# Optimization experiments

Measured on AMD Instinct MI355X. Metric: run time of the kernel, lower is better.

Reference implementation:

```python
import jax, jax.numpy as jnp
import numpy as np

N = 50000      # n_nodes
E = 800000     # n_edges (avg degree 16)
D_IN, D_HID, D_OUT = 128, 128, 64


def setup_inputs() -> dict:
    key = jax.random.key(0)
    ks = jax.random.split(key, 6)
    x = jax.random.normal(ks[0], (N, D_IN), dtype=jnp.float32)
    edge_index = jax.random.randint(ks[1], (2, E), 0, N, dtype=jnp.int32)
    # GCNConv params (glorot-ish scale), bias enabled by default in PyG
    W1 = jax.random.normal(ks[2], (D_IN, D_HID), dtype=jnp.float32) * (1.0 / np.sqrt(D_IN))
    b1 = jnp.zeros((D_HID,), dtype=jnp.float32)
    W2 = jax.random.normal(ks[3], (D_HID, D_OUT), dtype=jnp.float32) * (1.0 / np.sqrt(D_HID))
    b2 = jnp.zeros((D_OUT,), dtype=jnp.float32)
    return {"x": x, "edge_index": edge_index, "W1": W1, "b1": b1, "W2": W2, "b2": b2}


def _gcn_conv(x, src, dst, W, b):
    """PyG GCNConv: linear transform, add self-loops (weight 1),
    symmetric D^-1/2 A D^-1/2 aggregation (source->target), add bias."""
    xw = x @ W                                                # [N, Dout]
    ones = jnp.ones(dst.shape[0], dtype=xw.dtype)
    deg = jax.ops.segment_sum(ones, dst, num_segments=N) + 1.0  # +1 self-loop
    dis = jax.lax.rsqrt(deg)                                  # deg >= 1
    norm = dis[src] * dis[dst]                                # [E]
    msg = xw[src] * norm[:, None]                             # gather + scale
    agg = jax.ops.segment_sum(msg, dst, num_segments=N)       # scatter-add
    agg = agg + xw * (dis * dis)[:, None]                     # self-loop term
    return agg + b


def reference(x, edge_index, W1, b1, W2, b2):
    src, dst = edge_index[0], edge_index[1]
    z = jax.nn.relu(_gcn_conv(x, src, dst, W1, b1))
    z = _gcn_conv(z, src, dst, W2, b2)
    return z
```

## Files before the change

### kernel.cpp

```cpp
#include <hip/hip_runtime.h>

#define NN 50000
#define NE 800000
#define NB 196
#define BCAP 4608
#define KPAD 136
#define WSLAB (2 * 64 * KPAD)
#define CHUNKS 782

typedef __bf16 bf16x8 __attribute__((ext_vector_type(8)));
typedef float  f32x4  __attribute__((ext_vector_type(4)));

static __device__ __forceinline__ float bf2f(unsigned short h){
  union { unsigned u; float f; } c; c.u = ((unsigned)h) << 16; return c.f;
}
static __device__ __forceinline__ unsigned short f2bf(float f){
  union { float f; unsigned u; } c; c.f = f;
  unsigned u = c.u;
  return (unsigned short)((u + 0x7fffu + ((u >> 16) & 1u)) >> 16);
}
static __device__ __forceinline__ void split8(const float* f, bf16x8& hi, bf16x8& lo){
  #pragma unroll
  for (int j = 0; j < 8; j++){
    __bf16 h = (__bf16)f[j];
    hi[j] = h;
    lo[j] = (__bf16)(f[j] - (float)h);
  }
}
static __device__ __forceinline__ void addu4(float* a, uint4 w){
  a[0] += bf2f((unsigned short)(w.x & 0xffffu)); a[1] += bf2f((unsigned short)(w.x >> 16));
  a[2] += bf2f((unsigned short)(w.y & 0xffffu)); a[3] += bf2f((unsigned short)(w.y >> 16));
  a[4] += bf2f((unsigned short)(w.z & 0xffffu)); a[5] += bf2f((unsigned short)(w.z >> 16));
  a[6] += bf2f((unsigned short)(w.w & 0xffffu)); a[7] += bf2f((unsigned short)(w.w >> 16));
}

__global__ __launch_bounds__(256) void k_prep(const float* __restrict__ W1,
    const float* __restrict__ W2, unsigned short* __restrict__ wbuf,
    int* __restrict__ gcur){
  int s = blockIdx.x;
  if (s == 3){
    if (threadIdx.x < NB) gcur[threadIdx.x] = 0;
    return;
  }
  const float* W = (s < 2) ? W1 : W2;
  int ldw = (s < 2) ? 128 : 64;
  int coff = (s == 1) ? 64 : 0;
  unsigned short* wh = wbuf + (size_t)s * WSLAB;
  unsigned short* wl = wh + 64 * KPAD;
  for (int i = threadIdx.x; i < 128 * 64; i += 256){
    int k = i >> 6, n = i & 63;
    float v = W[(size_t)k * ldw + coff + n];
    unsigned short h = f2bf(v);
    unsigned short l = f2bf(v - bf2f(h));
    wh[n * KPAD + k] = h;
    wl[n * KPAD + k] = l;
  }
}

__global__ __launch_bounds__(256) void k_bfill(const int* __restrict__ src,
    const int* __restrict__ dst, int* __restrict__ gcur, unsigned* __restrict__ stg){
  __shared__ int lcnt[NB];
  __shared__ int gbase[NB];
  for (int i = threadIdx.x; i < NB; i += 256) lcnt[i] = 0;
  __syncthreads();
  int per = (NE + gridDim.x - 1) / gridDim.x;
  int e0 = blockIdx.x * per, e1 = min(e0 + per, NE);
  for (int e = e0 + threadIdx.x; e < e1; e += 256)
    atomicAdd(&lcnt[dst[e] >> 8], 1);
  __syncthreads();
  for (int b = threadIdx.x; b < NB; b += 256){
    gbase[b] = atomicAdd(&gcur[b], lcnt[b]);
    lcnt[b] = 0;
  }
  __syncthreads();
  for (int e = e0 + threadIdx.x; e < e1; e += 256){
    int d = dst[e];
    int b = d >> 8;
    unsigned entry = (unsigned)src[e] | (((unsigned)d & 255u) << 16);
    int pos = gbase[b] + atomicAdd(&lcnt[b], 1);
    if (pos < BCAP) stg[(size_t)b * BCAP + pos] = entry;
  }
}

__global__ __launch_bounds__(256) void k_build(const unsigned* __restrict__ stg,
    const int* __restrict__ gcur, int* __restrict__ rowstart, int* __restrict__ cnt,
    float* __restrict__ dis, int* __restrict__ csr){
  __shared__ int lcnt[256];
  __shared__ int sm[256];
  const int b = blockIdx.x;
  const int t = threadIdx.x;
  const int ecnt = min(gcur[b], BCAP);
  const int ebase = b * BCAP;
  lcnt[t] = 0;
  __syncthreads();
  for (int i = t; i < ecnt; i += 256){
    unsigned en = stg[ebase + i];
    atomicAdd(&lcnt[(en >> 16) & 255u], 1);
  }
  __syncthreads();
  int v = lcnt[t];
  sm[t] = v;
  __syncthreads();
  #pragma unroll
  for (int off = 1; off < 256; off <<= 1){
    int x = (t >= off) ? sm[t - off] : 0;
    __syncthreads();
    sm[t] += x;
    __syncthreads();
  }
  const int loff = sm[t] - v;
  const int node = (b << 8) + t;
  if (node < NN){
    rowstart[node] = ebase + loff;
    cnt[node] = v;
    dis[node] = rsqrtf((float)v + 1.0f);
  }
  __syncthreads();
  lcnt[t] = loff;
  __syncthreads();
  for (int i = t; i < ecnt; i += 256){
    unsigned en = stg[ebase + i];
    int pos = atomicAdd(&lcnt[(en >> 16) & 255u], 1);
    csr[ebase + pos] = (int)(en & 0xffffu);
  }
}

__global__ __launch_bounds__(256) void k_gemm1(const float* __restrict__ X,
    const unsigned short* __restrict__ wbuf, const float* __restrict__ dis,
    unsigned short* __restrict__ Y){
  const int t = threadIdx.x;
  const int wv = t >> 6;
  const int lane = t & 63;
  const int m = lane & 15;
  const int quad = lane >> 4;
  const int R0 = blockIdx.x * 64;
  const int row = R0 + wv * 16 + m;
  const int rowc = min(row, NN - 1);
  const float* pX = X + (size_t)rowc * 128 + quad * 8;

  f32x4 acc[8];
  #pragma unroll
  for (int tt = 0; tt < 8; tt++) acc[tt] = (f32x4){0.f, 0.f, 0.f, 0.f};

  #pragma unroll
  for (int ki = 0; ki < 4; ki++){
    float a[8];
    *(float4*)(a)     = *(const float4*)(pX + ki * 32);
    *(float4*)(a + 4) = *(const float4*)(pX + ki * 32 + 4);
    bf16x8 ah, al;
    split8(a, ah, al);
    #pragma unroll
    for (int tt = 0; tt < 8; tt++){
      const unsigned short* bp = wbuf + (tt >> 2) * WSLAB
                               + ((tt & 3) * 16 + m) * KPAD + ki * 32 + quad * 8;
      bf16x8 bh = *(const bf16x8*)bp;
      bf16x8 bl = *(const bf16x8*)(bp + 64 * KPAD);
      acc[tt] = __builtin_amdgcn_mfma_f32_16x16x32_bf16(ah, bh, acc[tt], 0, 0, 0);
      acc[tt] = __builtin_amdgcn_mfma_f32_16x16x32_bf16(ah, bl, acc[tt], 0, 0, 0);
      acc[tt] = __builtin_amdgcn_mfma_f32_16x16x32_bf16(al, bh, acc[tt], 0, 0, 0);
    }
  }

  const int orow = R0 + wv * 16 + quad * 4;
  #pragma unroll
  for (int r = 0; r < 4; r++){
    int gr = orow + r;
    if (gr < NN){
      float dsc = dis[gr];
      #pragma unroll
      for (int tt = 0; tt < 8; tt++)
        Y[(size_t)gr * 128 + (tt >> 2) * 64 + (tt & 3) * 16 + m] = f2bf(acc[tt][r] * dsc);
    }
  }
}

__global__ __launch_bounds__(256) void k_gemm2(const unsigned short* __restrict__ Ah,
    const unsigned short* __restrict__ Wsl, const float* __restrict__ dis,
    unsigned short* __restrict__ Y){
  const int t = threadIdx.x;
  const int wv = t >> 6;
  const int lane = t & 63;
  const int m = lane & 15;
  const int quad = lane >> 4;
  const int R0 = blockIdx.x * 64;
  const int row = R0 + wv * 16 + m;
  const int rowc = min(row, NN - 1);
  const unsigned short* pAh = Ah + (size_t)rowc * 128 + quad * 8;

  f32x4 acc[4];
  #pragma unroll
  for (int tt = 0; tt < 4; tt++) acc[tt] = (f32x4){0.f, 0.f, 0.f, 0.f};

  #pragma unroll
  for (int ki = 0; ki < 4; ki++){
    bf16x8 ah = *(const bf16x8*)(pAh + ki * 32);
    #pragma unroll
    for (int tt = 0; tt < 4; tt++){
      const unsigned short* bp = Wsl + (tt * 16 + m) * KPAD + ki * 32 + quad * 8;
      bf16x8 bh = *(const bf16x8*)bp;
      bf16x8 bl = *(const bf16x8*)(bp + 64 * KPAD);
      acc[tt] = __builtin_amdgcn_mfma_f32_16x16x32_bf16(ah, bh, acc[tt], 0, 0, 0);
      acc[tt] = __builtin_amdgcn_mfma_f32_16x16x32_bf16(ah, bl, acc[tt], 0, 0, 0);
    }
  }

  const int orow = R0 + wv * 16 + quad * 4;
  #pragma unroll
  for (int r = 0; r < 4; r++){
    int gr = orow + r;
    if (gr < NN){
      float dsc = dis[gr];
      #pragma unroll
      for (int tt = 0; tt < 4; tt++)
        Y[(size_t)gr * 64 + tt * 16 + m] = f2bf(acc[tt][r] * dsc);
    }
  }
}

__global__ __launch_bounds__(256) void k_agg1(const unsigned short* __restrict__ Y,
    const int* __restrict__ rowstart, const int* __restrict__ cnt,
    const int* __restrict__ csr, const float* __restrict__ dis,
    const float* __restrict__ bias, unsigned short* __restrict__ OH){
  const int n = (blockIdx.x * 256 + threadIdx.x) >> 6;
  const int lane = threadIdx.x & 63;
  const int q = lane >> 4;
  const int l = lane & 15;
  if (n >= NN) return;
  float a[8] = {0.f, 0.f, 0.f, 0.f, 0.f, 0.f, 0.f, 0.f};
  if (q == 0)
    addu4(a, *(const uint4*)(Y + (size_t)n * 128 + (l << 3)));
  const int start = rowstart[n];
  const int end = start + cnt[n];
  int i = start;
  for (; i + 16 <= end; i += 16){
    int s0 = csr[i + q],     s1 = csr[i + 4 + q];
    int s2 = csr[i + 8 + q], s3 = csr[i + 12 + q];
    uint4 w0 = *(const uint4*)(Y + (size_t)s0 * 128 + (l << 3));
    uint4 w1 = *(const uint4*)(Y + (size_t)s1 * 128 + (l << 3));
    uint4 w2 = *(const uint4*)(Y + (size_t)s2 * 128 + (l << 3));
    uint4 w3 = *(const uint4*)(Y + (size_t)s3 * 128 + (l << 3));
    addu4(a, w0); addu4(a, w1); addu4(a, w2); addu4(a, w3);
  }
  for (; i + 8 <= end; i += 8){
    int s0 = csr[i + q], s1 = csr[i + 4 + q];
    uint4 w0 = *(const uint4*)(Y + (size_t)s0 * 128 + (l << 3));
    uint4 w1 = *(const uint4*)(Y + (size_t)s1 * 128 + (l << 3));
    addu4(a, w0); addu4(a, w1);
  }
  for (; i < end; i += 4){
    int idx = i + q;
    if (idx < end){
      int s = csr[idx];
      addu4(a, *(const uint4*)(Y + (size_t)s * 128 + (l << 3)));
    }
  }
  #pragma unroll
  for (int j = 0; j < 8; j++){
    a[j] += __shfl_xor(a[j], 16);
    a[j] += __shfl_xor(a[j], 32);
  }
  if (q == 0){
    const float dn = dis[n];
    float bi[8];
    *(float4*)(bi)     = *(const float4*)(bias + (l << 3));
    *(float4*)(bi + 4) = *(const float4*)(bias + (l << 3) + 4);
    unsigned hv[4];
    #pragma unroll
    for (int j = 0; j < 4; j++){
      float o0 = fmaxf(dn * a[2 * j]     + bi[2 * j],     0.f);
      float o1 = fmaxf(dn * a[2 * j + 1] + bi[2 * j + 1], 0.f);
      hv[j] = (unsigned)f2bf(o0) | ((unsigned)f2bf(o1) << 16);
    }
    *(uint4*)(OH + (size_t)n * 128 + (l << 3)) = make_uint4(hv[0], hv[1], hv[2], hv[3]);
  }
}

__global__ __launch_bounds__(256) void k_agg64(const unsigned short* __restrict__ Y,
    const int* __restrict__ rowstart, const int* __restrict__ cnt,
    const int* __restrict__ csr, const float* __restrict__ dis,
    const float* __restrict__ bias, float* __restrict__ OUT){
  const int n = (blockIdx.x * 256 + threadIdx.x) >> 6;
  const int lane = threadIdx.x & 63;
  const int g = lane >> 3;
  const int l = lane & 7;
  if (n >= NN) return;
  float a[8] = {0.f, 0.f, 0.f, 0.f, 0.f, 0.f, 0.f, 0.f};
  if (g == 0)
    addu4(a, *(const uint4*)(Y + (size_t)n * 64 + (l << 3)));
  const int start = rowstart[n];
  const int end = start + cnt[n];
  int i = start;
  for (; i + 16 <= end; i += 16){
    int s0 = csr[i + g], s1 = csr[i + 8 + g];
    uint4 w0 = *(const uint4*)(Y + (size_t)s0 * 64 + (l << 3));
    uint4 w1 = *(const uint4*)(Y + (size_t)s1 * 64 + (l << 3));
    addu4(a, w0); addu4(a, w1);
  }
  for (; i < end; i += 8){
    int idx = i + g;
    if (idx < end){
      int s = csr[idx];
      addu4(a, *(const uint4*)(Y + (size_t)s * 64 + (l << 3)));
    }
  }
  #pragma unroll
  for (int j = 0; j < 8; j++){
    a[j] += __shfl_xor(a[j], 8);
    a[j] += __shfl_xor(a[j], 16);
    a[j] += __shfl_xor(a[j], 32);
  }
  if (g == 0){
    const float dn = dis[n];
    float bi[8];
    *(float4*)(bi)     = *(const float4*)(bias + (l << 3));
    *(float4*)(bi + 4) = *(const float4*)(bias + (l << 3) + 4);
    float4 o0, o1;
    o0.x = dn * a[0] + bi[0]; o0.y = dn * a[1] + bi[1];
    o0.z = dn * a[2] + bi[2]; o0.w = dn * a[3] + bi[3];
    o1.x = dn * a[4] + bi[4]; o1.y = dn * a[5] + bi[5];
    o1.z = dn * a[6] + bi[6]; o1.w = dn * a[7] + bi[7];
    *(float4*)(OUT + (size_t)n * 64 + (l << 3))     = o0;
    *(float4*)(OUT + (size_t)n * 64 + (l << 3) + 4) = o1;
  }
}

extern "C" void kernel_launch(void* const* d_in, const int* in_sizes, int n_in,
                              void* d_out, int out_size, void* d_ws, size_t ws_size,
                              hipStream_t stream) {
  const float* x  = (const float*)d_in[0];
  const int*   ei = (const int*)d_in[1];
  const int*   src = ei;
  const int*   dst = ei + NE;
  const float* W1 = (const float*)d_in[2];
  const float* b1 = (const float*)d_in[3];
  const float* W2 = (const float*)d_in[4];
  const float* b2 = (const float*)d_in[5];
  float* out = (float*)d_out;

  char* w = (char*)d_ws;
  auto alloc = [&](size_t bytes){ void* p = (void*)w; w += (bytes + 255) & ~(size_t)255; return p; };
  int*   gcur     = (int*)alloc(NB * 4);
  int*   rowstart = (int*)alloc((size_t)NN * 4);
  int*   cnt      = (int*)alloc((size_t)NN * 4);
  float* dis      = (float*)alloc((size_t)NN * 4);
  unsigned* stg   = (unsigned*)alloc((size_t)NB * BCAP * 4);
  int*   csr      = (int*)alloc((size_t)NB * BCAP * 4);
  unsigned short* y1 = (unsigned short*)alloc((size_t)NN * 128 * 2);
  unsigned short* hh = (unsigned short*)alloc((size_t)NN * 128 * 2);
  unsigned short* y2 = (unsigned short*)alloc((size_t)NN * 64 * 2);
  unsigned short* wbuf = (unsigned short*)alloc((size_t)3 * WSLAB * 2);

  const int AGG_BLOCKS = (NN * 64 + 255) / 256;
  unsigned short* wsl2 = wbuf + (size_t)2 * WSLAB;

  k_prep <<<4, 256, 0, stream>>>(W1, W2, wbuf, gcur);
  k_bfill<<<256, 256, 0, stream>>>(src, dst, gcur, stg);
  k_build<<<NB, 256, 0, stream>>>(stg, gcur, rowstart, cnt, dis, csr);

  k_gemm1<<<CHUNKS, 256, 0, stream>>>(x, wbuf, dis, y1);
  k_agg1 <<<AGG_BLOCKS, 256, 0, stream>>>(y1, rowstart, cnt, csr, dis, b1, hh);
  k_gemm2<<<CHUNKS, 256, 0, stream>>>(hh, wsl2, dis, y2);
  k_agg64<<<AGG_BLOCKS, 256, 0, stream>>>(y2, rowstart, cnt, csr, dis, b2, out);
}
```

Measured before the change: 212.2 us.

## Overlap first-layer GEMM with graph build by merging into bucket-fill and build kernels

The first GEMM no longer depends on the degree normalization, because the source-side scale is moved into the aggregation as a per-neighbor dis[src] multiply. Its chunks are then split between the bucket-fill and CSR-build kernels as extra blocks, so the dense matmul runs alongside the irregular graph preprocessing and one launch is removed. In exchange, agg1 performs an extra dis gather and an FMA per neighbor, and y1 is stored in bf16 without the scale applied, which slightly changes rounding.

```diff
diff --git a/kernel.cpp b/kernel.cpp
--- a/kernel.cpp
+++ b/kernel.cpp
@@ -7,6 +7,8 @@
 #define KPAD 136
 #define WSLAB (2 * 64 * KPAD)
 #define CHUNKS 782
+#define G1A 391
+#define NBF 256
 
 typedef __bf16 bf16x8 __attribute__((ext_vector_type(8)));
 typedef float  f32x4  __attribute__((ext_vector_type(4)));
@@ -26,6 +28,16 @@
     hi[j] = h;
     lo[j] = (__bf16)(f[j] - (float)h);
   }
+}
+static __device__ __forceinline__ void addu4s(float* a, uint4 w, float s){
+  a[0] = fmaf(s, bf2f((unsigned short)(w.x & 0xffffu)), a[0]);
+  a[1] = fmaf(s, bf2f((unsigned short)(w.x >> 16)),     a[1]);
+  a[2] = fmaf(s, bf2f((unsigned short)(w.y & 0xffffu)), a[2]);
+  a[3] = fmaf(s, bf2f((unsigned short)(w.y >> 16)),     a[3]);
+  a[4] = fmaf(s, bf2f((unsigned short)(w.z & 0xffffu)), a[4]);
+  a[5] = fmaf(s, bf2f((unsigned short)(w.z >> 16)),     a[5]);
+  a[6] = fmaf(s, bf2f((unsigned short)(w.w & 0xffffu)), a[6]);
+  a[7] = fmaf(s, bf2f((unsigned short)(w.w >> 16)),     a[7]);
 }
 static __device__ __forceinline__ void addu4(float* a, uint4 w){
   a[0] += bf2f((unsigned short)(w.x & 0xffffu)); a[1] += bf2f((unsigned short)(w.x >> 16));
@@ -34,106 +46,14 @@
   a[6] += bf2f((unsigned short)(w.w & 0xffffu)); a[7] += bf2f((unsigned short)(w.w >> 16));
 }
 
-__global__ __launch_bounds__(256) void k_prep(const float* __restrict__ W1,
-    const float* __restrict__ W2, unsigned short* __restrict__ wbuf,
-    int* __restrict__ gcur){
-  int s = blockIdx.x;
-  if (s == 3){
-    if (threadIdx.x < NB) gcur[threadIdx.x] = 0;
-    return;
-  }
-  const float* W = (s < 2) ? W1 : W2;
-  int ldw = (s < 2) ? 128 : 64;
-  int coff = (s == 1) ? 64 : 0;
-  unsigned short* wh = wbuf + (size_t)s * WSLAB;
-  unsigned short* wl = wh + 64 * KPAD;
-  for (int i = threadIdx.x; i < 128 * 64; i += 256){
-    int k = i >> 6, n = i & 63;
-    float v = W[(size_t)k * ldw + coff + n];
-    unsigned short h = f2bf(v);
-    unsigned short l = f2bf(v - bf2f(h));
-    wh[n * KPAD + k] = h;
-    wl[n * KPAD + k] = l;
-  }
-}
-
-__global__ __launch_bounds__(256) void k_bfill(const int* __restrict__ src,
-    const int* __restrict__ dst, int* __restrict__ gcur, unsigned* __restrict__ stg){
-  __shared__ int lcnt[NB];
-  __shared__ int gbase[NB];
-  for (int i = threadIdx.x; i < NB; i += 256) lcnt[i] = 0;
-  __syncthreads();
-  int per = (NE + gridDim.x - 1) / gridDim.x;
-  int e0 = blockIdx.x * per, e1 = min(e0 + per, NE);
-  for (int e = e0 + threadIdx.x; e < e1; e += 256)
-    atomicAdd(&lcnt[dst[e] >> 8], 1);
-  __syncthreads();
-  for (int b = threadIdx.x; b < NB; b += 256){
-    gbase[b] = atomicAdd(&gcur[b], lcnt[b]);
-    lcnt[b] = 0;
-  }
-  __syncthreads();
-  for (int e = e0 + threadIdx.x; e < e1; e += 256){
-    int d = dst[e];
-    int b = d >> 8;
-    unsigned entry = (unsigned)src[e] | (((unsigned)d & 255u) << 16);
-    int pos = gbase[b] + atomicAdd(&lcnt[b], 1);
-    if (pos < BCAP) stg[(size_t)b * BCAP + pos] = entry;
-  }
-}
-
-__global__ __launch_bounds__(256) void k_build(const unsigned* __restrict__ stg,
-    const int* __restrict__ gcur, int* __restrict__ rowstart, int* __restrict__ cnt,
-    float* __restrict__ dis, int* __restrict__ csr){
-  __shared__ int lcnt[256];
-  __shared__ int sm[256];
-  const int b = blockIdx.x;
-  const int t = threadIdx.x;
-  const int ecnt = min(gcur[b], BCAP);
-  const int ebase = b * BCAP;
-  lcnt[t] = 0;
-  __syncthreads();
-  for (int i = t; i < ecnt; i += 256){
-    unsigned en = stg[ebase + i];
-    atomicAdd(&lcnt[(en >> 16) & 255u], 1);
-  }
-  __syncthreads();
-  int v = lcnt[t];
-  sm[t] = v;
-  __syncthreads();
-  #pragma unroll
-  for (int off = 1; off < 256; off <<= 1){
-    int x = (t >= off) ? sm[t - off] : 0;
-    __syncthreads();
-    sm[t] += x;
-    __syncthreads();
-  }
-  const int loff = sm[t] - v;
-  const int node = (b << 8) + t;
-  if (node < NN){
-    rowstart[node] = ebase + loff;
-    cnt[node] = v;
-    dis[node] = rsqrtf((float)v + 1.0f);
-  }
-  __syncthreads();
-  lcnt[t] = loff;
-  __syncthreads();
-  for (int i = t; i < ecnt; i += 256){
-    unsigned en = stg[ebase + i];
-    int pos = atomicAdd(&lcnt[(en >> 16) & 255u], 1);
-    csr[ebase + pos] = (int)(en & 0xffffu);
-  }
-}
-
-__global__ __launch_bounds__(256) void k_gemm1(const float* __restrict__ X,
-    const unsigned short* __restrict__ wbuf, const float* __restrict__ dis,
+static __device__ __forceinline__ void gemm1_body(int chunk, int t,
+    const float* __restrict__ X, const unsigned short* __restrict__ wbuf,
     unsigned short* __restrict__ Y){
-  const int t = threadIdx.x;
   const int wv = t >> 6;
   const int lane = t & 63;
   const int m = lane & 15;
   const int quad = lane >> 4;
-  const int R0 = blockIdx.x * 64;
+  const int R0 = chunk * 64;
   const int row = R0 + wv * 16 + m;
   const int rowc = min(row, NN - 1);
   const float* pX = X + (size_t)rowc * 128 + quad * 8;
@@ -166,11 +86,176 @@
   for (int r = 0; r < 4; r++){
     int gr = orow + r;
     if (gr < NN){
-      float dsc = dis[gr];
       #pragma unroll
       for (int tt = 0; tt < 8; tt++)
-        Y[(size_t)gr * 128 + (tt >> 2) * 64 + (tt & 3) * 16 + m] = f2bf(acc[tt][r] * dsc);
-    }
+        Y[(size_t)gr * 128 + (tt >> 2) * 64 + (tt & 3) * 16 + m] = f2bf(acc[tt][r]);
+    }
+  }
+}
+
+__global__ __launch_bounds__(256) void k_prep(const float* __restrict__ W1,
+    const float* __restrict__ W2, unsigned short* __restrict__ wbuf,
+    int* __restrict__ gcur){
+  int s = blockIdx.x;
+  if (s == 3){
+    if (threadIdx.x < NB) gcur[threadIdx.x] = 0;
+    return;
+  }
+  const float* W = (s < 2) ? W1 : W2;
+  int ldw = (s < 2) ? 128 : 64;
+  int coff = (s == 1) ? 64 : 0;
+  unsigned short* wh = wbuf + (size_t)s * WSLAB;
+  unsigned short* wl = wh + 64 * KPAD;
+  for (int i = threadIdx.x; i < 128 * 64; i += 256){
+    int k = i >> 6, n = i & 63;
+    float v = W[(size_t)k * ldw + coff + n];
+    unsigned short h = f2bf(v);
+    unsigned short l = f2bf(v - bf2f(h));
+    wh[n * KPAD + k] = h;
+    wl[n * KPAD + k] = l;
+  }
+}
+
+__global__ __launch_bounds__(256) void k_fg1(const int* __restrict__ src,
+    const int* __restrict__ dst, int* __restrict__ gcur, unsigned* __restrict__ stg,
+    const float* __restrict__ X, const unsigned short* __restrict__ wbuf,
+    unsigned short* __restrict__ Y){
+  const int bid = blockIdx.x;
+  const int t = threadIdx.x;
+  if (bid >= NBF){
+    gemm1_body(bid - NBF, t, X, wbuf, Y);
+    return;
+  }
+  __shared__ int lcnt[NB];
+  __shared__ int gbase[NB];
+  for (int i = t; i < NB; i += 256) lcnt[i] = 0;
+  __syncthreads();
+  const int per = (NE + NBF - 1) / NBF;
+  const int e0 = bid * per, e1 = min(e0 + per, NE);
+  for (int e = e0 + t; e < e1; e += 256)
+    atomicAdd(&lcnt[dst[e] >> 8], 1);
+  __syncthreads();
+  for (int b = t; b < NB; b += 256){
+    gbase[b] = atomicAdd(&gcur[b], lcnt[b]);
+    lcnt[b] = 0;
+  }
+  __syncthreads();
+  for (int e = e0 + t; e < e1; e += 256){
+    int d = dst[e];
+    int b = d >> 8;
+    unsigned entry = (unsigned)src[e] | (((unsigned)d & 255u) << 16);
+    int pos = gbase[b] + atomicAdd(&lcnt[b], 1);
+    if (pos < BCAP) stg[(size_t)b * BCAP + pos] = entry;
+  }
+}
+
+__global__ __launch_bounds__(256) void k_bg1(const unsigned* __restrict__ stg,
+    const int* __restrict__ gcur, int* __restrict__ rowstart, int* __restrict__ cnt,
+    float* __restrict__ dis, int* __restrict__ csr,
+    const float* __restrict__ X, const unsigned short* __restrict__ wbuf,
+    unsigned short* __restrict__ Y){
+  const int bid = blockIdx.x;
+  const int t = threadIdx.x;
+  if (bid >= NB){
+    gemm1_body(G1A + (bid - NB), t, X, wbuf, Y);
+    return;
+  }
+  __shared__ int lcnt[256];
+  __shared__ int sm[256];
+  const int b = bid;
+  const int ecnt = min(gcur[b], BCAP);
+  const int ebase = b * BCAP;
+  lcnt[t] = 0;
+  __syncthreads();
+  for (int i = t; i < ecnt; i += 256){
+    unsigned en = stg[ebase + i];
+    atomicAdd(&lcnt[(en >> 16) & 255u], 1);
+  }
+  __syncthreads();
+  int v = lcnt[t];
+  sm[t] = v;
+  __syncthreads();
+  #pragma unroll
+  for (int off = 1; off < 256; off <<= 1){
+    int x = (t >= off) ? sm[t - off] : 0;
+    __syncthreads();
+    sm[t] += x;
+    __syncthreads();
+  }
+  const int loff = sm[t] - v;
+  const int node = (b << 8) + t;
+  if (node < NN){
+    rowstart[node] = ebase + loff;
+    cnt[node] = v;
+    dis[node] = rsqrtf((float)v + 1.0f);
+  }
+  __syncthreads();
+  lcnt[t] = loff;
+  __syncthreads();
+  for (int i = t; i < ecnt; i += 256){
+    unsigned en = stg[ebase + i];
+    int pos = atomicAdd(&lcnt[(en >> 16) & 255u], 1);
+    csr[ebase + pos] = (int)(en & 0xffffu);
+  }
+}
+
+__global__ __launch_bounds__(256) void k_agg1(const unsigned short* __restrict__ Y,
+    const int* __restrict__ rowstart, const int* __restrict__ cnt,
+    const int* __restrict__ csr, const float* __restrict__ dis,
+    const float* __restrict__ bias, unsigned short* __restrict__ OH){
+  const int n = (blockIdx.x * 256 + threadIdx.x) >> 6;
+  const int lane = threadIdx.x & 63;
+  const int q = lane >> 4;
+  const int l = lane & 15;
+  if (n >= NN) return;
+  const float dn = dis[n];
+  float a[8] = {0.f, 0.f, 0.f, 0.f, 0.f, 0.f, 0.f, 0.f};
+  if (q == 0)
+    addu4s(a, *(const uint4*)(Y + (size_t)n * 128 + (l << 3)), dn);
+  const int start = rowstart[n];
+  const int end = start + cnt[n];
+  int i = start;
+  for (; i + 16 <= end; i += 16){
+    int s0 = csr[i + q],     s1 = csr[i + 4 + q];
+    int s2 = csr[i + 8 + q], s3 = csr[i + 12 + q];
+    float d0 = dis[s0], d1 = dis[s1], d2 = dis[s2], d3 = dis[s3];
+    uint4 w0 = *(const uint4*)(Y + (size_t)s0 * 128 + (l << 3));
+    uint4 w1 = *(const uint4*)(Y + (size_t)s1 * 128 + (l << 3));
+    uint4 w2 = *(const uint4*)(Y + (size_t)s2 * 128 + (l << 3));
+    uint4 w3 = *(const uint4*)(Y + (size_t)s3 * 128 + (l << 3));
+    addu4s(a, w0, d0); addu4s(a, w1, d1); addu4s(a, w2, d2); addu4s(a, w3, d3);
+  }
+  for (; i + 8 <= end; i += 8){
+    int s0 = csr[i + q], s1 = csr[i + 4 + q];
+    float d0 = dis[s0], d1 = dis[s1];
+    uint4 w0 = *(const uint4*)(Y + (size_t)s0 * 128 + (l << 3));
+    uint4 w1 = *(const uint4*)(Y + (size_t)s1 * 128 + (l << 3));
+    addu4s(a, w0, d0); addu4s(a, w1, d1);
+  }
+  for (; i < end; i += 4){
+    int idx = i + q;
+    if (idx < end){
+      int s = csr[idx];
+      addu4s(a, *(const uint4*)(Y + (size_t)s * 128 + (l << 3)), dis[s]);
+    }
+  }
+  #pragma unroll
+  for (int j = 0; j < 8; j++){
+    a[j] += __shfl_xor(a[j], 16);
+    a[j] += __shfl_xor(a[j], 32);
+  }
+  if (q == 0){
+    float bi[8];
+    *(float4*)(bi)     = *(const float4*)(bias + (l << 3));
+    *(float4*)(bi + 4) = *(const float4*)(bias + (l << 3) + 4);
+    unsigned hv[4];
+    #pragma unroll
+    for (int j = 0; j < 4; j++){
+      float o0 = fmaxf(dn * a[2 * j]     + bi[2 * j],     0.f);
+      float o1 = fmaxf(dn * a[2 * j + 1] + bi[2 * j + 1], 0.f);
+      hv[j] = (unsigned)f2bf(o0) | ((unsigned)f2bf(o1) << 16);
+    }
+    *(uint4*)(OH + (size_t)n * 128 + (l << 3)) = make_uint4(hv[0], hv[1], hv[2], hv[3]);
   }
 }
 
@@ -214,64 +299,6 @@
       for (int tt = 0; tt < 4; tt++)
         Y[(size_t)gr * 64 + tt * 16 + m] = f2bf(acc[tt][r] * dsc);
     }
-  }
-}
-
-__global__ __launch_bounds__(256) void k_agg1(const unsigned short* __restrict__ Y,
-    const int* __restrict__ rowstart, const int* __restrict__ cnt,
-    const int* __restrict__ csr, const float* __restrict__ dis,
-    const float* __restrict__ bias, unsigned short* __restrict__ OH){
-  const int n = (blockIdx.x * 256 + threadIdx.x) >> 6;
-  const int lane = threadIdx.x & 63;
-  const int q = lane >> 4;
-  const int l = lane & 15;
-  if (n >= NN) return;
-  float a[8] = {0.f, 0.f, 0.f, 0.f, 0.f, 0.f, 0.f, 0.f};
-  if (q == 0)
-    addu4(a, *(const uint4*)(Y + (size_t)n * 128 + (l << 3)));
-  const int start = rowstart[n];
-  const int end = start + cnt[n];
-  int i = start;
-  for (; i + 16 <= end; i += 16){
-    int s0 = csr[i + q],     s1 = csr[i + 4 + q];
-    int s2 = csr[i + 8 + q], s3 = csr[i + 12 + q];
-    uint4 w0 = *(const uint4*)(Y + (size_t)s0 * 128 + (l << 3));
-    uint4 w1 = *(const uint4*)(Y + (size_t)s1 * 128 + (l << 3));
-    uint4 w2 = *(const uint4*)(Y + (size_t)s2 * 128 + (l << 3));
-    uint4 w3 = *(const uint4*)(Y + (size_t)s3 * 128 + (l << 3));
-    addu4(a, w0); addu4(a, w1); addu4(a, w2); addu4(a, w3);
-  }
-  for (; i + 8 <= end; i += 8){
-    int s0 = csr[i + q], s1 = csr[i + 4 + q];
-    uint4 w0 = *(const uint4*)(Y + (size_t)s0 * 128 + (l << 3));
-    uint4 w1 = *(const uint4*)(Y + (size_t)s1 * 128 + (l << 3));
-    addu4(a, w0); addu4(a, w1);
-  }
-  for (; i < end; i += 4){
-    int idx = i + q;
-    if (idx < end){
-      int s = csr[idx];
-      addu4(a, *(const uint4*)(Y + (size_t)s * 128 + (l << 3)));
-    }
-  }
-  #pragma unroll
-  for (int j = 0; j < 8; j++){
-    a[j] += __shfl_xor(a[j], 16);
-    a[j] += __shfl_xor(a[j], 32);
-  }
-  if (q == 0){
-    const float dn = dis[n];
-    float bi[8];
-    *(float4*)(bi)     = *(const float4*)(bias + (l << 3));
-    *(float4*)(bi + 4) = *(const float4*)(bias + (l << 3) + 4);
-    unsigned hv[4];
-    #pragma unroll
-    for (int j = 0; j < 4; j++){
-      float o0 = fmaxf(dn * a[2 * j]     + bi[2 * j],     0.f);
-      float o1 = fmaxf(dn * a[2 * j + 1] + bi[2 * j + 1], 0.f);
-      hv[j] = (unsigned)f2bf(o0) | ((unsigned)f2bf(o1) << 16);
-    }
-    *(uint4*)(OH + (size_t)n * 128 + (l << 3)) = make_uint4(hv[0], hv[1], hv[2], hv[3]);
   }
 }
 
@@ -353,11 +380,10 @@
   const int AGG_BLOCKS = (NN * 64 + 255) / 256;
   unsigned short* wsl2 = wbuf + (size_t)2 * WSLAB;
 
-  k_prep <<<4, 256, 0, stream>>>(W1, W2, wbuf, gcur);
-  k_bfill<<<256, 256, 0, stream>>>(src, dst, gcur, stg);
-  k_build<<<NB, 256, 0, stream>>>(stg, gcur, rowstart, cnt, dis, csr);
-
-  k_gemm1<<<CHUNKS, 256, 0, stream>>>(x, wbuf, dis, y1);
+  k_prep<<<4, 256, 0, stream>>>(W1, W2, wbuf, gcur);
+  k_fg1 <<<NBF + G1A, 256, 0, stream>>>(src, dst, gcur, stg, x, wbuf, y1);
+  k_bg1 <<<NB + (CHUNKS - G1A), 256, 0, stream>>>(stg, gcur, rowstart, cnt, dis, csr,
+                                                  x, wbuf, y1);
   k_agg1 <<<AGG_BLOCKS, 256, 0, stream>>>(y1, rowstart, cnt, csr, dis, b1, hh);
   k_gemm2<<<CHUNKS, 256, 0, stream>>>(hh, wsl2, dis, y2);
   k_agg64<<<AGG_BLOCKS, 256, 0, stream>>>(y2, rowstart, cnt, csr, dis, b2, out);
```

Result: faster. 193.4 us (-8.9%).
